# Kernel optimization log

Measured on AMD Instinct MI355X. Metric: run time of the kernel, lower is better.

Reference implementation:

```python
import jax, jax.numpy as jnp
import numpy as np

B, T, V, R = 512, 24, 32000, 32
# Scale keeps both the selected chain (factor ~ sqrt(R)*c per step) and the
# vocab-marginalized chain (factor ~ sqrt(V*R)*c per step) inside fp32 range.
CORE_SCALE = (R * np.sqrt(V)) ** -0.5


def setup_inputs() -> dict:
    key = jax.random.key(0)
    k1, k2, k3, k4 = jax.random.split(key, 4)
    y = jax.random.randint(k1, (B, T), 0, V)                      # (B, T) token ids
    alpha = jax.random.normal(k2, (1, R), dtype=jnp.float32)      # left boundary
    beta = jax.random.normal(k3, (1, R), dtype=jnp.float32)       # right boundary
    core = jax.random.normal(k4, (1, R, V, R), dtype=jnp.float32) * CORE_SCALE
    return {"y": y, "alpha": alpha, "beta": beta, "core": core}


def _mps_fwd(alpha, beta, core, y):
    a = alpha[0]                                   # (R,)
    b = beta[0]                                    # (R,)
    cores = jnp.transpose(core[0], (1, 0, 2))      # (V, R, R): per-token transfer matrices
    bsz, seq = y.shape

    # --- unnormalized p(y): chain of selected R x R matrices (marginalize_mask = 0) ---
    sel = jnp.moveaxis(cores[y], 1, 0)             # (T, B, R, R) gathered transfer matrices
    init = jnp.broadcast_to(a, (bsz, R))           # (B, R)

    def step(state, M):                            # state: (B, R), M: (B, R, R)
        return jnp.einsum('br,brs->bs', state, M), None

    state, _ = jax.lax.scan(step, init, sel)
    p_tilde = state @ b                            # (B,)

    # --- normalization: every position marginalized over vocab (free pos-0 leg also summed) ---
    m = cores.sum(axis=0)                          # (R, R) marginalized transfer matrix

    def zstep(v, _):                               # v: (R,)
        return v @ m, None

    vz, _ = jax.lax.scan(zstep, a, None, length=seq)
    z = (vz @ b) * bsz                             # z_one is identical per row; .sum() over batch

    return jnp.concatenate([p_tilde, z[None]])     # (B + 1,): [p_tilde..., z]


def reference(y, alpha, beta, core):
    return _mps_fwd(alpha, beta, core, y)
```

## Files before the change

kernel.cpp:

```cpp
#include <hip/hip_runtime.h>

#define RNK 32
#define VOC 32000
#define BSZ 512
#define SEQ 24

#define CHAIN_BLOCKS 128
#define REDUCE_BLOCKS 4000

typedef const __attribute__((address_space(1))) void* as1_cvp;
typedef __attribute__((address_space(3))) void* as3_vp;

__device__ __forceinline__ void issue_matrix_load(const float* __restrict__ src_tok,
                                                  float* lds_base, int lane) {
    const int r  = lane >> 3;
    const int c0 = (lane & 7) * 4;
    #pragma unroll
    for (int j = 0; j < 4; ++j) {
        const float* src = src_tok + (size_t)(j * 8 + r) * ((size_t)VOC * RNK) + c0;
        __builtin_amdgcn_global_load_lds((as1_cvp)src, (as3_vp)(lds_base + j * 256), 16, 0, 0);
    }
}

__global__ __launch_bounds__(256) void fused_kernel(const float* __restrict__ core,
                                                    const int* __restrict__ y,
                                                    const float* __restrict__ alpha,
                                                    const float* __restrict__ beta,
                                                    float* __restrict__ out,
                                                    float* __restrict__ gm) {
    __shared__ float shmem[4 * 3 * 1024 + RNK];

    if (blockIdx.x < CHAIN_BLOCKS) {
        const int tid  = threadIdx.x;
        const int lane = tid & 63;
        const int w    = tid >> 6;
        const int s    = lane & 31;
        const int half = lane >> 5;
        const int row  = blockIdx.x * 4 + w;

        float* mybuf = shmem + w * 3072;

        int   ytok  = (lane < SEQ) ? y[row * SEQ + lane] : 0;
        float state = alpha[s];
        float betav = beta[s];

        asm volatile("s_waitcnt vmcnt(0)" ::: "memory");

        {
            const int tok = __shfl(ytok, 0, 64);
            issue_matrix_load(core + (size_t)tok * RNK, mybuf + 0 * 1024, lane);
        }
        {
            const int tok = __shfl(ytok, 1, 64);
            issue_matrix_load(core + (size_t)tok * RNK, mybuf + 1 * 1024, lane);
        }

        #pragma unroll
        for (int t = 0; t < SEQ; ++t) {
            if (t < SEQ - 1) asm volatile("s_waitcnt vmcnt(4)" ::: "memory");
            else             asm volatile("s_waitcnt vmcnt(0)" ::: "memory");
            __builtin_amdgcn_sched_barrier(0);

            if (t + 2 < SEQ) {
                const int tok = __shfl(ytok, t + 2, 64);
                issue_matrix_load(core + (size_t)tok * RNK, mybuf + ((t + 2) % 3) * 1024, lane);
            }

            const float* M = mybuf + (t % 3) * 1024;
            float a0 = 0.f, a1 = 0.f, a2 = 0.f, a3 = 0.f;
            #pragma unroll
            for (int i = 0; i < 16; i += 4) {
                a0 = fmaf(__shfl(state, half * 16 + i + 0, 64), M[(half * 16 + i + 0) * 32 + s], a0);
                a1 = fmaf(__shfl(state, half * 16 + i + 1, 64), M[(half * 16 + i + 1) * 32 + s], a1);
                a2 = fmaf(__shfl(state, half * 16 + i + 2, 64), M[(half * 16 + i + 2) * 32 + s], a2);
                a3 = fmaf(__shfl(state, half * 16 + i + 3, 64), M[(half * 16 + i + 3) * 32 + s], a3);
            }
            const float acc = (a0 + a1) + (a2 + a3);
            state = acc + __shfl_xor(acc, 32, 64);
        }

        float p = state * betav;
        #pragma unroll
        for (int m = 16; m >= 1; m >>= 1) p += __shfl_xor(p, m, 64);
        if (lane == 0) out[row] = p;
    } else {
        const int bid   = blockIdx.x - CHAIN_BLOCKS;
        const int r     = bid & 31;
        const int chunk = bid >> 5;
        const int tid   = threadIdx.x;

        const float4* slab = (const float4*)(core + (size_t)r * VOC * RNK);
        const int base = chunk * 2048 + tid;

        float a0 = 0.f, a1 = 0.f, a2 = 0.f, a3 = 0.f;
        #pragma unroll
        for (int i = 0; i < 8; ++i) {
            float4 v = slab[base + i * 256];
            a0 += v.x; a1 += v.y; a2 += v.z; a3 += v.w;
        }

        float* ml = shmem;
        if (tid < RNK) ml[tid] = 0.f;
        __syncthreads();

        const int s0 = (tid & 7) * 4;
        atomicAdd(&ml[s0 + 0], a0);
        atomicAdd(&ml[s0 + 1], a1);
        atomicAdd(&ml[s0 + 2], a2);
        atomicAdd(&ml[s0 + 3], a3);
        __syncthreads();

        if (tid < RNK) atomicAdd(&gm[r * RNK + tid], ml[tid]);
    }
}

__global__ void zchain_kernel(const float* __restrict__ gm,
                              const float* __restrict__ alpha,
                              const float* __restrict__ beta,
                              float* __restrict__ out) {
    const int lane = threadIdx.x & 63;
    const int s    = lane & 31;
    const int half = lane >> 5;

    float col[16];
    #pragma unroll
    for (int i = 0; i < 16; ++i) col[i] = gm[(half * 16 + i) * RNK + s];

    float v = alpha[s];
    #pragma unroll
    for (int t = 0; t < SEQ; ++t) {
        float a0 = 0.f, a1 = 0.f, a2 = 0.f, a3 = 0.f;
        #pragma unroll
        for (int i = 0; i < 16; i += 4) {
            a0 = fmaf(__shfl(v, half * 16 + i + 0, 64), col[i + 0], a0);
            a1 = fmaf(__shfl(v, half * 16 + i + 1, 64), col[i + 1], a1);
            a2 = fmaf(__shfl(v, half * 16 + i + 2, 64), col[i + 2], a2);
            a3 = fmaf(__shfl(v, half * 16 + i + 3, 64), col[i + 3], a3);
        }
        const float acc = (a0 + a1) + (a2 + a3);
        v = acc + __shfl_xor(acc, 32, 64);
    }
    float z = v * beta[s];
    #pragma unroll
    for (int m = 16; m >= 1; m >>= 1) z += __shfl_xor(z, m, 64);
    if (lane == 0) out[BSZ] = z * (float)BSZ;
}

extern "C" void kernel_launch(void* const* d_in, const int* in_sizes, int n_in,
                              void* d_out, int out_size, void* d_ws, size_t ws_size,
                              hipStream_t stream) {
    const int*   y     = (const int*)d_in[0];
    const float* alpha = (const float*)d_in[1];
    const float* beta  = (const float*)d_in[2];
    const float* core  = (const float*)d_in[3];
    float* out = (float*)d_out;
    float* gm  = (float*)d_ws;

    hipMemsetAsync(gm, 0, RNK * RNK * sizeof(float), stream);
    fused_kernel<<<CHAIN_BLOCKS + REDUCE_BLOCKS, 256, 0, stream>>>(core, y, alpha, beta, out, gm);
    zchain_kernel<<<1, 64, 0, stream>>>(gm, alpha, beta, out);
}
```

Measured before the change: 48.40 us.

## Deepen chain prefetch pipeline to six stages and halve block size

Each chain wave now prefetches six gathered transfer matrices into LDS ahead of use instead of two, with per-step vmcnt waits adjusted to match the deeper queue. Blocks shrink to 128 threads (two chains per block, 256 chain blocks), and each reduce thread sums 16 float4s with a 128 stride so the per-block coverage of the core slab stays the same. The goal is to hide more gather latency in the serial 24-step chain and to give finer-grained blocks for scheduling. The cost is more LDS per wave (six 4 KB buffers) and hand-tuned waitcnt values that depend on each load issuing exactly four instructions.

```diff
diff --git a/kernel.cpp b/kernel.cpp
--- a/kernel.cpp
+++ b/kernel.cpp
@@ -5,13 +5,15 @@
 #define BSZ 512
 #define SEQ 24
 
-#define CHAIN_BLOCKS 128
+#define BLOCK 128
+#define CHAIN_BLOCKS 256
 #define REDUCE_BLOCKS 4000
+#define DEPTH 6
 
 typedef const __attribute__((address_space(1))) void* as1_cvp;
 typedef __attribute__((address_space(3))) void* as3_vp;
 
-__device__ __forceinline__ void issue_matrix_load(const float* __restrict__ src_tok,
+__device__ __forceinline__ void issue_matrix_load(const float* src_tok,
                                                   float* lds_base, int lane) {
     const int r  = lane >> 3;
     const int c0 = (lane & 7) * 4;
@@ -22,13 +24,13 @@
     }
 }
 
-__global__ __launch_bounds__(256) void fused_kernel(const float* __restrict__ core,
-                                                    const int* __restrict__ y,
-                                                    const float* __restrict__ alpha,
-                                                    const float* __restrict__ beta,
-                                                    float* __restrict__ out,
-                                                    float* __restrict__ gm) {
-    __shared__ float shmem[4 * 3 * 1024 + RNK];
+__global__ __launch_bounds__(BLOCK) void fused_kernel(const float* __restrict__ core,
+                                                      const int* __restrict__ y,
+                                                      const float* __restrict__ alpha,
+                                                      const float* __restrict__ beta,
+                                                      float* __restrict__ out,
+                                                      float* __restrict__ gm) {
+    __shared__ float shmem[2 * DEPTH * 1024 + RNK];
 
     if (blockIdx.x < CHAIN_BLOCKS) {
         const int tid  = threadIdx.x;
@@ -36,9 +38,9 @@
         const int w    = tid >> 6;
         const int s    = lane & 31;
         const int half = lane >> 5;
-        const int row  = blockIdx.x * 4 + w;
+        const int row  = blockIdx.x * 2 + w;
 
-        float* mybuf = shmem + w * 3072;
+        float* mybuf = shmem + w * (DEPTH * 1024);
 
         int   ytok  = (lane < SEQ) ? y[row * SEQ + lane] : 0;
         float state = alpha[s];
@@ -46,27 +48,29 @@
 
         asm volatile("s_waitcnt vmcnt(0)" ::: "memory");
 
-        {
-            const int tok = __shfl(ytok, 0, 64);
-            issue_matrix_load(core + (size_t)tok * RNK, mybuf + 0 * 1024, lane);
-        }
-        {
-            const int tok = __shfl(ytok, 1, 64);
-            issue_matrix_load(core + (size_t)tok * RNK, mybuf + 1 * 1024, lane);
+        #pragma unroll
+        for (int pt = 0; pt < DEPTH; ++pt) {
+            const int tok = __shfl(ytok, pt, 64);
+            issue_matrix_load(core + (size_t)tok * RNK, mybuf + pt * 1024, lane);
         }
 
         #pragma unroll
         for (int t = 0; t < SEQ; ++t) {
-            if (t < SEQ - 1) asm volatile("s_waitcnt vmcnt(4)" ::: "memory");
-            else             asm volatile("s_waitcnt vmcnt(0)" ::: "memory");
+            if      (t <= SEQ - DEPTH) asm volatile("s_waitcnt vmcnt(20)" ::: "memory");
+            else if (t == SEQ - 5)     asm volatile("s_waitcnt vmcnt(16)" ::: "memory");
+            else if (t == SEQ - 4)     asm volatile("s_waitcnt vmcnt(12)" ::: "memory");
+            else if (t == SEQ - 3)     asm volatile("s_waitcnt vmcnt(8)"  ::: "memory");
+            else if (t == SEQ - 2)     asm volatile("s_waitcnt vmcnt(4)"  ::: "memory");
+            else                       asm volatile("s_waitcnt vmcnt(0)"  ::: "memory");
             __builtin_amdgcn_sched_barrier(0);
 
-            if (t + 2 < SEQ) {
-                const int tok = __shfl(ytok, t + 2, 64);
-                issue_matrix_load(core + (size_t)tok * RNK, mybuf + ((t + 2) % 3) * 1024, lane);
+            if (t + DEPTH < SEQ) {
+                const int tok = __shfl(ytok, t + DEPTH, 64);
+                issue_matrix_load(core + (size_t)tok * RNK,
+                                  mybuf + ((t + DEPTH) % DEPTH) * 1024, lane);
             }
 
-            const float* M = mybuf + (t % 3) * 1024;
+            const float* M = mybuf + (t % DEPTH) * 1024;
             float a0 = 0.f, a1 = 0.f, a2 = 0.f, a3 = 0.f;
             #pragma unroll
             for (int i = 0; i < 16; i += 4) {
@@ -94,8 +98,8 @@
 
         float a0 = 0.f, a1 = 0.f, a2 = 0.f, a3 = 0.f;
         #pragma unroll
-        for (int i = 0; i < 8; ++i) {
-            float4 v = slab[base + i * 256];
+        for (int i = 0; i < 16; ++i) {
+            float4 v = slab[base + i * 128];
             a0 += v.x; a1 += v.y; a2 += v.z; a3 += v.w;
         }
 
@@ -157,6 +161,6 @@
     float* gm  = (float*)d_ws;
 
     hipMemsetAsync(gm, 0, RNK * RNK * sizeof(float), stream);
-    fused_kernel<<<CHAIN_BLOCKS + REDUCE_BLOCKS, 256, 0, stream>>>(core, y, alpha, beta, out, gm);
+    fused_kernel<<<CHAIN_BLOCKS + REDUCE_BLOCKS, BLOCK, 0, stream>>>(core, y, alpha, beta, out, gm);
     zchain_kernel<<<1, 64, 0, stream>>>(gm, alpha, beta, out);
 }
```

Measured after the change: 42.33 us. 1.14x faster.
